# Performance work log

Hardware: AMD Instinct MI355X
Metric: run time of the kernel (lower is better)

The kernel has to match this reference:

```python
import jax, jax.numpy as jnp
import numpy as np

K = 512           # num_embeddings
D = 256           # embedding_dim
GRID = (16, 32)   # SOM grid, prod == K
SIGMA = 2.0       # Gaussian neighborhood width (blur at step 0)
COMMITMENT_COST = 0.25
KOHONEN_COST = 1.0


def _make_blur_matrix():
    # Grid.init id->coord: coord[j] = (i // prod(shape[:j])) % shape[j]
    idx = np.arange(K)
    c0 = idx % GRID[0]
    c1 = (idx // GRID[0]) % GRID[1]
    coords = np.stack([c0, c1], axis=-1).astype(np.float32)  # [K, 2]
    dist = np.linalg.norm(coords[None, :, :] - coords[:, None, :], axis=-1)  # [K, K]
    return jnp.asarray(np.exp(-(dist ** 2) / (2.0 * SIGMA ** 2)), dtype=jnp.float32)


def setup_inputs() -> dict:
    key = jax.random.key(0)
    kx, kw = jax.random.split(key)
    x = jax.random.normal(kx, (64, 32, 32, D), dtype=jnp.float32)
    w = jax.random.normal(kw, (K, D), dtype=jnp.float32)
    bmat = _make_blur_matrix()  # [K, K] constant buffer
    return {"x": x, "w": w, "bmat": bmat}


def reference(x, w, bmat):
    sg = jax.lax.stop_gradient
    flat = x.reshape(-1, D)  # [N, D]

    # nearest-code search (no_grad in torch)
    fw = sg(flat)
    ww = sg(w)
    dists = (jnp.sum(fw ** 2, axis=1, keepdims=True)
             + jnp.sum(ww ** 2, axis=1)
             - 2.0 * fw @ ww.T)                       # [N, K]
    enc_idx = jnp.argmin(dists, axis=1)               # [N]
    encodings = jax.nn.one_hot(enc_idx, K, dtype=jnp.float32)  # [N, K]

    # embedding lookup (differentiable w.r.t. w)
    quant_flat = w[enc_idx]                           # [N, D]
    quantized = quant_flat.reshape(x.shape)

    # l2_batch(w, quantized.detach()) -> [N, K]
    qd = sg(quant_flat)
    diff = (jnp.sum(w ** 2, axis=1)[None, :]
            + jnp.sum(qd ** 2, axis=1, keepdims=True)
            - 2.0 * qd @ w.T)                         # [N, K]

    # blur-weighted kohonen loss: bmm(diff[N,1,K], bmat[idx][N,K,1]).mean()
    selected = bmat[enc_idx]                          # [N, K]
    kohonen_loss = jnp.mean(jnp.sum(diff * selected, axis=-1))

    avg_probs = jnp.mean(encodings, axis=0)
    perplexity = jnp.exp(-jnp.sum(avg_probs * jnp.log(avg_probs + 1e-10)))

    e_latent = jnp.mean((sg(quantized) - x) ** 2)
    q_latent = jnp.mean((quantized - sg(x)) ** 2)
    loss = q_latent + COMMITMENT_COST * e_latent + KOHONEN_COST * kohonen_loss

    quantized_st = x + sg(quantized - x)              # straight-through
    return loss, quantized_st, perplexity, enc_idx
```

## Files before the change

### kernel.cpp

```cpp
#include <hip/hip_runtime.h>
#include <hip/hip_bf16.h>
#include <hip/hip_fp16.h>
#include <math.h>

#define NPTS 65536
#define DIM  256
#define KC   512

#define BM    64
#define NBLK  (NPTS / BM)
#define XSTR  264
#define EPS   0.01f

#define QOFF  1
#define PIDX  16777217
#define EOFF  16777218


typedef _Float16 h8    __attribute__((ext_vector_type(8)));
typedef float    f32x4 __attribute__((ext_vector_type(4)));

__device__ inline void cvt_split8(float4 a, float4 b, h8& hv, h8& lv) {
    float f[8] = {a.x, a.y, a.z, a.w, b.x, b.y, b.z, b.w};
    #pragma unroll
    for (int i = 0; i < 8; ++i) {
        _Float16 h = (_Float16)f[i];
        hv[i] = h;
        lv[i] = (_Float16)(f[i] - (float)h);
    }
}

__device__ inline void gload16(const _Float16* gp, _Float16* lp) {
    __builtin_amdgcn_global_load_lds(
        (const __attribute__((address_space(1))) void*)gp,
        (__attribute__((address_space(3))) void*)lp, 16, 0, 0);
}

__device__ inline void merge_top2(float& b1, int& i1, float& b2, int& i2,
                                  float ob1, int oi1, float ob2, int oi2) {
    bool ow = (ob1 < b1) || (ob1 == b1 && oi1 < i1);
    float lb = ow ? b1 : ob1; int li = ow ? i1 : oi1;
    if (ow) { b1 = ob1; i1 = oi1; }
    float c2 = b2; int ci = i2;
    if (ob2 < c2 || (ob2 == c2 && oi2 < ci)) { c2 = ob2; ci = oi2; }
    if (lb  < c2 || (lb  == c2 && li  < ci)) { c2 = lb;  ci = li;  }
    b2 = c2; i2 = ci;
}

__device__ inline float exact_dist(const float* __restrict__ xr,
                                   const float* __restrict__ w, int c, float wsqc) {
    const float* wr = w + (size_t)c * DIM;
    float d0 = 0.f, d1 = 0.f, d2 = 0.f, d3 = 0.f;
    #pragma unroll 4
    for (int d = 0; d < DIM; d += 4) {
        d0 = fmaf(xr[d + 0], wr[d + 0], d0);
        d1 = fmaf(xr[d + 1], wr[d + 1], d1);
        d2 = fmaf(xr[d + 2], wr[d + 2], d2);
        d3 = fmaf(xr[d + 3], wr[d + 3], d3);
    }
    return wsqc - 2.f * ((d0 + d1) + (d2 + d3));
}

__global__ __launch_bounds__(256) void som_wsq(const float* __restrict__ w,
                                               float* __restrict__ wsq,
                                               int* __restrict__ hist,
                                               double* __restrict__ mse_acc)
{
    int k = blockIdx.x * 256 + threadIdx.x;
    const float4* r = reinterpret_cast<const float4*>(w + (size_t)k * DIM);
    float s0 = 0.f, s1 = 0.f, s2 = 0.f, s3 = 0.f;
    #pragma unroll 8
    for (int q = 0; q < DIM / 4; ++q) {
        float4 v = r[q];
        s0 = fmaf(v.x, v.x, s0);
        s1 = fmaf(v.y, v.y, s1);
        s2 = fmaf(v.z, v.z, s2);
        s3 = fmaf(v.w, v.w, s3);
    }
    wsq[k] = (s0 + s1) + (s2 + s3);
    hist[k] = 0;
    if (k == 0) *mse_acc = 0.0;
}

__global__ __launch_bounds__(256) void som_conv(const float* __restrict__ w,
                                                _Float16* __restrict__ wfh,
                                                _Float16* __restrict__ wfl)
{
    const int tid = threadIdx.x;
    const int row = blockIdx.x * 8 + (tid >> 5);
    const int g   = tid & 31;
    const float4* r = reinterpret_cast<const float4*>(w + (size_t)row * DIM);
    float4 a = r[g * 2], b = r[g * 2 + 1];
    h8 hv, lv; cvt_split8(a, b, hv, lv);
    int dsl = g >> 2, kg = g & 3;
    size_t off = ((size_t)(dsl * 32 + (row >> 4))) * 512 + kg * 128 + (row & 15) * 8;
    *reinterpret_cast<h8*>(wfh + off) = hv;
    *reinterpret_cast<h8*>(wfl + off) = lv;
}

__global__ __launch_bounds__(512) void som_main(const float* __restrict__ x,
                                                const float* __restrict__ w,
                                                const _Float16* __restrict__ wfh,
                                                const _Float16* __restrict__ wfl,
                                                float* __restrict__ out,
                                                const float* __restrict__ wsq,
                                                int* __restrict__ hist,
                                                double* __restrict__ mse_acc)
{
    alignas(16) __shared__ _Float16 AsH[16384];
    alignas(16) __shared__ _Float16 AsL[16384];
    alignas(16) __shared__ _Float16 xh[BM * XSTR];
    alignas(16) __shared__ _Float16 xl[BM * XSTR];
    __shared__ float wsq_s[KC];
    __shared__ float xsq_s[BM];
    __shared__ float red_b[8][BM], red_s[8][BM];
    __shared__ int   red_ib[8][BM], red_is[8][BM];
    __shared__ int   bidx_s[BM];

    const int tid  = threadIdx.x;
    const int lane = tid & 63;
    const int wid  = tid >> 6;
    const int l15  = lane & 15;
    const int kg   = lane >> 4;
    const int ptBlock = blockIdx.x * BM;

    const float4* xg4 = reinterpret_cast<const float4*>(x);
    #pragma unroll
    for (int it = 0; it < 4; ++it) {
        int u = it * 512 + tid, row = u >> 5, c8 = u & 31;
        float4 a = xg4[(size_t)(ptBlock + row) * 64 + c8 * 2];
        float4 b = xg4[(size_t)(ptBlock + row) * 64 + c8 * 2 + 1];
        h8 hv, lv; cvt_split8(a, b, hv, lv);
        *reinterpret_cast<h8*>(&xh[row * XSTR + c8 * 8]) = hv;
        *reinterpret_cast<h8*>(&xl[row * XSTR + c8 * 8]) = lv;
        float s = ((fmaf(a.x, a.x, a.y * a.y) + fmaf(a.z, a.z, a.w * a.w))
                 + (fmaf(b.x, b.x, b.y * b.y) + fmaf(b.z, b.z, b.w * b.w)));
        #pragma unroll
        for (int m = 1; m <= 16; m <<= 1) s += __shfl_xor(s, m, 64);
        if ((lane & 31) == 0) xsq_s[row] = s;
    }
    wsq_s[tid] = wsq[tid];

    const int codeBase = wid * 64;
    const int ctg0 = wid * 4;

    f32x4 acc[4][4];
    #pragma unroll
    for (int rt = 0; rt < 4; ++rt)
        #pragma unroll
        for (int ct = 0; ct < 4; ++ct)
            acc[rt][ct] = (f32x4){0.f, 0.f, 0.f, 0.f};

    #pragma unroll 1
    for (int dsl = 0; dsl < 8; ++dsl) {
        #pragma unroll
        for (int i = 0; i < 4; ++i) {
            size_t goff = (size_t)dsl * 16384 + (size_t)(i * 512 + tid) * 8;
            int loff = (i * 512 + wid * 64) * 8;
            gload16(wfh + goff, &AsH[loff]);
            gload16(wfl + goff, &AsL[loff]);
        }
        __syncthreads();

        h8 Bh[4], Bl[4];
        #pragma unroll
        for (int ct = 0; ct < 4; ++ct) {
            int boff = (ct * 16 + l15) * XSTR + dsl * 32 + kg * 8;
            Bh[ct] = *reinterpret_cast<const h8*>(&xh[boff]);
            Bl[ct] = *reinterpret_cast<const h8*>(&xl[boff]);
        }
        #pragma unroll
        for (int rt = 0; rt < 4; ++rt) {
            int aoff = (ctg0 + rt) * 512 + kg * 128 + l15 * 8;
            h8 Ah = *reinterpret_cast<const h8*>(&AsH[aoff]);
            h8 Al = *reinterpret_cast<const h8*>(&AsL[aoff]);
            #pragma unroll
            for (int ct = 0; ct < 4; ++ct)
                acc[rt][ct] = __builtin_amdgcn_mfma_f32_16x16x32_f16(Ah, Bh[ct], acc[rt][ct], 0, 0, 0);
            #pragma unroll
            for (int ct = 0; ct < 4; ++ct)
                acc[rt][ct] = __builtin_amdgcn_mfma_f32_16x16x32_f16(Al, Bh[ct], acc[rt][ct], 0, 0, 0);
            #pragma unroll
            for (int ct = 0; ct < 4; ++ct)
                acc[rt][ct] = __builtin_amdgcn_mfma_f32_16x16x32_f16(Ah, Bl[ct], acc[rt][ct], 0, 0, 0);
        }
        __syncthreads();
    }

    float sb[4], ss[4];
    int   ib[4], is2[4];
    #pragma unroll
    for (int ct = 0; ct < 4; ++ct) { sb[ct] = INFINITY; ss[ct] = INFINITY; ib[ct] = 0; is2[ct] = 0; }
    #pragma unroll
    for (int rt = 0; rt < 4; ++rt) {
        int cbase = codeBase + rt * 16 + kg * 4;
        #pragma unroll
        for (int ct = 0; ct < 4; ++ct) {
            #pragma unroll
            for (int r = 0; r < 4; ++r) {
                int cc = cbase + r;
                float d = wsq_s[cc] - 2.f * acc[rt][ct][r];
                if (d < sb[ct] || (d == sb[ct] && cc < ib[ct])) {
                    ss[ct] = sb[ct]; is2[ct] = ib[ct]; sb[ct] = d; ib[ct] = cc;
                } else if (d < ss[ct] || (d == ss[ct] && cc < is2[ct])) {
                    ss[ct] = d; is2[ct] = cc;
                }
            }
        }
    }
    #pragma unroll
    for (int ct = 0; ct < 4; ++ct) {
        #pragma unroll
        for (int m = 16; m <= 32; m <<= 1) {
            float ob1 = __shfl_xor(sb[ct], m, 64), ob2 = __shfl_xor(ss[ct], m, 64);
            int   oi1 = __shfl_xor(ib[ct], m, 64), oi2 = __shfl_xor(is2[ct], m, 64);
            merge_top2(sb[ct], ib[ct], ss[ct], is2[ct], ob1, oi1, ob2, oi2);
        }
    }
    if (kg == 0) {
        #pragma unroll
        for (int ct = 0; ct < 4; ++ct) {
            int p = ct * 16 + l15;
            red_b[wid][p] = sb[ct];  red_s[wid][p] = ss[ct];
            red_ib[wid][p] = ib[ct]; red_is[wid][p] = is2[ct];
        }
    }
    __syncthreads();

    if (tid < BM) {
        float b = red_b[0][tid], s = red_s[0][tid];
        int  bi = red_ib[0][tid], si = red_is[0][tid];
        #pragma unroll
        for (int g = 1; g < 8; ++g)
            merge_top2(b, bi, s, si, red_b[g][tid], red_ib[g][tid], red_s[g][tid], red_is[g][tid]);

        if (s - b < EPS) {
            const float* xrp = x + (size_t)(ptBlock + tid) * DIM;
            float d1 = exact_dist(xrp, w, bi, wsq_s[bi]);
            float d2 = exact_dist(xrp, w, si, wsq_s[si]);
            if (d2 < d1 || (d2 == d1 && si < bi)) { bi = si; b = d2; } else { b = d1; }
        }
        bidx_s[tid] = bi;
        out[EOFF + ptBlock + tid] = (float)bi;
        atomicAdd(&hist[bi], 1);

        float msum = xsq_s[tid] + b;
        #pragma unroll
        for (int m = 32; m; m >>= 1) msum += __shfl_xor(msum, m, 64);
        if (tid == 0) atomicAdd(mse_acc, (double)msum);
    }
    __syncthreads();

    {
        const float4* wg4 = reinterpret_cast<const float4*>(w);
        float4* q4 = reinterpret_cast<float4*>(out + QOFF);
        #pragma unroll
        for (int r8 = 0; r8 < 8; ++r8) {
            int row = r8 * 8 + wid;
            int cc = bidx_s[row];
            q4[(size_t)(ptBlock + row) * 64 + lane] = wg4[(size_t)cc * 64 + lane];
        }
    }
}

__global__ __launch_bounds__(256) void som_g(const float* __restrict__ w,
                                             const float* __restrict__ bmat,
                                             const float* __restrict__ wsq,
                                             float* __restrict__ g)
{
    __shared__ float wj[DIM];
    __shared__ float psum[4];
    const int j = blockIdx.x;
    const int tid = threadIdx.x;
    wj[tid] = w[(size_t)j * DIM + tid];
    __syncthreads();
    const float wsqj = wsq[j];
    float sum = 0.f;
    for (int k = tid; k < KC; k += 256) {
        const float* wk = &w[(size_t)k * DIM];
        float d0 = 0.f, d1 = 0.f, d2 = 0.f, d3 = 0.f;
        #pragma unroll 4
        for (int d = 0; d < DIM; d += 4) {
            d0 = fmaf(wj[d + 0], wk[d + 0], d0);
            d1 = fmaf(wj[d + 1], wk[d + 1], d1);
            d2 = fmaf(wj[d + 2], wk[d + 2], d2);
            d3 = fmaf(wj[d + 3], wk[d + 3], d3);
        }
        float dot = (d0 + d1) + (d2 + d3);
        float t = wsq[k] + wsqj - 2.f * dot;
        sum = fmaf(bmat[(size_t)j * KC + k], t, sum);
    }
    #pragma unroll
    for (int m = 32; m; m >>= 1) sum += __shfl_xor(sum, m, 64);
    int lane = tid & 63, wid = tid >> 6;
    if (lane == 0) psum[wid] = sum;
    __syncthreads();
    if (tid == 0) g[j] = (psum[0] + psum[1]) + (psum[2] + psum[3]);
}

__global__ __launch_bounds__(512) void som_final(const int* __restrict__ hist,
                                                 const float* __restrict__ g,
                                                 const double* __restrict__ mse_acc,
                                                 float* __restrict__ out)
{
    __shared__ float e_part[8], k_part[8];
    const int tid = threadIdx.x;
    int cnt = hist[tid];
    float p = (float)cnt / (float)NPTS;
    float ent = -p * logf(p + 1e-10f);
    float koh = (float)cnt * g[tid];
    #pragma unroll
    for (int m = 32; m; m >>= 1) {
        ent += __shfl_xor(ent, m, 64);
        koh += __shfl_xor(koh, m, 64);
    }
    int lane = tid & 63, wid = tid >> 6;
    if (lane == 0) { e_part[wid] = ent; k_part[wid] = koh; }
    __syncthreads();
    if (tid == 0) {
        float es = 0.f, ks = 0.f;
        #pragma unroll
        for (int i = 0; i < 8; ++i) { es += e_part[i]; ks += k_part[i]; }
        float mse = (float)(*mse_acc / (double)(NPTS * (size_t)DIM));
        out[0] = fmaf(1.25f, mse, ks / (float)NPTS);
        out[PIDX] = expf(es);
    }
}

extern "C" void kernel_launch(void* const* d_in, const int* in_sizes, int n_in,
                              void* d_out, int out_size, void* d_ws, size_t ws_size,
                              hipStream_t stream) {
    const float* x    = (const float*)d_in[0];
    const float* w    = (const float*)d_in[1];
    const float* bmat = (const float*)d_in[2];
    float* out = (float*)d_out;

    _Float16* wfh = (_Float16*)d_ws;
    _Float16* wfl = wfh + 131072;
    float*  wsq  = (float*)((char*)d_ws + 524288);
    float*  g    = (float*)((char*)d_ws + 526336);
    int*    hist = (int*)((char*)d_ws + 528384);
    double* mse  = (double*)((char*)d_ws + 530432);

    som_wsq  <<<2, 256, 0, stream>>>(w, wsq, hist, mse);
    som_conv <<<64, 256, 0, stream>>>(w, wfh, wfl);
    som_main <<<NBLK, 512, 0, stream>>>(x, w, wfh, wfl, out, wsq, hist, mse);
    som_g    <<<KC, 256, 0, stream>>>(w, bmat, wsq, g);
    som_final<<<1, KC, 0, stream>>>(hist, g, mse, out);
}
```

Measured before the change: 191.0 us.

## Double point tile, stream codebook fragments from global, and split codes across waves

The point tile grows to 128 rows with 1024-thread blocks. The codebook hi/lo fp16 fragments are no longer staged into LDS via global_load_lds with barriers; each wave reads its A fragments directly from global/L2 in a relaid-out fragment order. Codes are processed in two passes of 256, so each wave holds fewer accumulators. Reduction buffers now alias the x tile in LDS. This removes per-slice syncs and LDS codebook traffic, but relies on L2 bandwidth for repeated codebook reads and halves the number of blocks.

Result: faster. 164.7 us (-13.8%).

```diff
diff --git a/kernel.cpp b/kernel.cpp
--- a/kernel.cpp
+++ b/kernel.cpp
@@ -7,7 +7,7 @@
 #define DIM  256
 #define KC   512
 
-#define BM    64
+#define BM    128
 #define NBLK  (NPTS / BM)
 #define XSTR  264
 #define EPS   0.01f
@@ -28,12 +28,6 @@
         hv[i] = h;
         lv[i] = (_Float16)(f[i] - (float)h);
     }
-}
-
-__device__ inline void gload16(const _Float16* gp, _Float16* lp) {
-    __builtin_amdgcn_global_load_lds(
-        (const __attribute__((address_space(1))) void*)gp,
-        (__attribute__((address_space(3))) void*)lp, 16, 0, 0);
 }
 
 __device__ inline void merge_top2(float& b1, int& i1, float& b2, int& i2,
@@ -93,41 +87,46 @@
     float4 a = r[g * 2], b = r[g * 2 + 1];
     h8 hv, lv; cvt_split8(a, b, hv, lv);
     int dsl = g >> 2, kg = g & 3;
-    size_t off = ((size_t)(dsl * 32 + (row >> 4))) * 512 + kg * 128 + (row & 15) * 8;
+    int ctg = row >> 4, l15 = row & 15;
+    size_t off = (((size_t)(ctg * 8 + dsl)) * 4 + kg) * 128 + l15 * 8;
     *reinterpret_cast<h8*>(wfh + off) = hv;
     *reinterpret_cast<h8*>(wfl + off) = lv;
 }
 
-__global__ __launch_bounds__(512) void som_main(const float* __restrict__ x,
-                                                const float* __restrict__ w,
-                                                const _Float16* __restrict__ wfh,
-                                                const _Float16* __restrict__ wfl,
-                                                float* __restrict__ out,
-                                                const float* __restrict__ wsq,
-                                                int* __restrict__ hist,
-                                                double* __restrict__ mse_acc)
-{
-    alignas(16) __shared__ _Float16 AsH[16384];
-    alignas(16) __shared__ _Float16 AsL[16384];
+__global__ __launch_bounds__(1024) void som_main(const float* __restrict__ x,
+                                                 const float* __restrict__ w,
+                                                 const _Float16* __restrict__ wfh,
+                                                 const _Float16* __restrict__ wfl,
+                                                 float* __restrict__ out,
+                                                 const float* __restrict__ wsq,
+                                                 int* __restrict__ hist,
+                                                 double* __restrict__ mse_acc)
+{
     alignas(16) __shared__ _Float16 xh[BM * XSTR];
     alignas(16) __shared__ _Float16 xl[BM * XSTR];
     __shared__ float wsq_s[KC];
     __shared__ float xsq_s[BM];
-    __shared__ float red_b[8][BM], red_s[8][BM];
-    __shared__ int   red_ib[8][BM], red_is[8][BM];
-    __shared__ int   bidx_s[BM];
+    __shared__ float wsum[2];
+
+    float* red_b  = reinterpret_cast<float*>(xh);
+    float* red_s  = red_b + 8 * BM;
+    int*   red_ib = reinterpret_cast<int*>(red_s + 8 * BM);
+    int*   red_is = red_ib + 8 * BM;
+    int*   bidx_s = reinterpret_cast<int*>(xl);
 
     const int tid  = threadIdx.x;
     const int lane = tid & 63;
     const int wid  = tid >> 6;
     const int l15  = lane & 15;
     const int kg   = lane >> 4;
+    const int pgrp = wid & 1;
+    const int cgrp = wid >> 1;
     const int ptBlock = blockIdx.x * BM;
 
     const float4* xg4 = reinterpret_cast<const float4*>(x);
     #pragma unroll
     for (int it = 0; it < 4; ++it) {
-        int u = it * 512 + tid, row = u >> 5, c8 = u & 31;
+        int u = it * 1024 + tid, row = u >> 5, c8 = u & 31;
         float4 a = xg4[(size_t)(ptBlock + row) * 64 + c8 * 2];
         float4 b = xg4[(size_t)(ptBlock + row) * 64 + c8 * 2 + 1];
         h8 hv, lv; cvt_split8(a, b, hv, lv);
@@ -139,75 +138,78 @@
         for (int m = 1; m <= 16; m <<= 1) s += __shfl_xor(s, m, 64);
         if ((lane & 31) == 0) xsq_s[row] = s;
     }
-    wsq_s[tid] = wsq[tid];
-
-    const int codeBase = wid * 64;
-    const int ctg0 = wid * 4;
-
-    f32x4 acc[4][4];
-    #pragma unroll
-    for (int rt = 0; rt < 4; ++rt)
-        #pragma unroll
-        for (int ct = 0; ct < 4; ++ct)
-            acc[rt][ct] = (f32x4){0.f, 0.f, 0.f, 0.f};
-
-    #pragma unroll 1
-    for (int dsl = 0; dsl < 8; ++dsl) {
-        #pragma unroll
-        for (int i = 0; i < 4; ++i) {
-            size_t goff = (size_t)dsl * 16384 + (size_t)(i * 512 + tid) * 8;
-            int loff = (i * 512 + wid * 64) * 8;
-            gload16(wfh + goff, &AsH[loff]);
-            gload16(wfl + goff, &AsL[loff]);
-        }
-        __syncthreads();
-
-        h8 Bh[4], Bl[4];
-        #pragma unroll
-        for (int ct = 0; ct < 4; ++ct) {
-            int boff = (ct * 16 + l15) * XSTR + dsl * 32 + kg * 8;
-            Bh[ct] = *reinterpret_cast<const h8*>(&xh[boff]);
-            Bl[ct] = *reinterpret_cast<const h8*>(&xl[boff]);
-        }
-        #pragma unroll
-        for (int rt = 0; rt < 4; ++rt) {
-            int aoff = (ctg0 + rt) * 512 + kg * 128 + l15 * 8;
-            h8 Ah = *reinterpret_cast<const h8*>(&AsH[aoff]);
-            h8 Al = *reinterpret_cast<const h8*>(&AsL[aoff]);
-            #pragma unroll
-            for (int ct = 0; ct < 4; ++ct)
-                acc[rt][ct] = __builtin_amdgcn_mfma_f32_16x16x32_f16(Ah, Bh[ct], acc[rt][ct], 0, 0, 0);
-            #pragma unroll
-            for (int ct = 0; ct < 4; ++ct)
-                acc[rt][ct] = __builtin_amdgcn_mfma_f32_16x16x32_f16(Al, Bh[ct], acc[rt][ct], 0, 0, 0);
-            #pragma unroll
-            for (int ct = 0; ct < 4; ++ct)
-                acc[rt][ct] = __builtin_amdgcn_mfma_f32_16x16x32_f16(Ah, Bl[ct], acc[rt][ct], 0, 0, 0);
-        }
-        __syncthreads();
-    }
+    if (tid < KC) wsq_s[tid] = wsq[tid];
+    __syncthreads();
 
     float sb[4], ss[4];
     int   ib[4], is2[4];
     #pragma unroll
     for (int ct = 0; ct < 4; ++ct) { sb[ct] = INFINITY; ss[ct] = INFINITY; ib[ct] = 0; is2[ct] = 0; }
-    #pragma unroll
-    for (int rt = 0; rt < 4; ++rt) {
-        int cbase = codeBase + rt * 16 + kg * 4;
-        #pragma unroll
-        for (int ct = 0; ct < 4; ++ct) {
+
+    #pragma unroll 1
+    for (int pass = 0; pass < 2; ++pass) {
+        f32x4 acc[2][4];
+        #pragma unroll
+        for (int rt = 0; rt < 2; ++rt)
+            #pragma unroll
+            for (int ct = 0; ct < 4; ++ct)
+                acc[rt][ct] = (f32x4){0.f, 0.f, 0.f, 0.f};
+
+        #pragma unroll 1
+        for (int dsl = 0; dsl < 8; ++dsl) {
+            int boff0 = (pgrp * 64 + l15) * XSTR + dsl * 32 + kg * 8;
+            h8 Bh[4];
+            #pragma unroll
+            for (int ct = 0; ct < 4; ++ct)
+                Bh[ct] = *reinterpret_cast<const h8*>(&xh[boff0 + ct * 16 * XSTR]);
+            h8 Ah[2], Al[2];
+            #pragma unroll
+            for (int rt = 0; rt < 2; ++rt) {
+                int ctg = pass * 16 + cgrp * 2 + rt;
+                size_t aoff = ((size_t)ctg * 8 + dsl) * 512 + kg * 128 + l15 * 8;
+                Ah[rt] = *reinterpret_cast<const h8*>(wfh + aoff);
+                Al[rt] = *reinterpret_cast<const h8*>(wfl + aoff);
+            }
+            #pragma unroll
+            for (int rt = 0; rt < 2; ++rt)
+                #pragma unroll
+                for (int ct = 0; ct < 4; ++ct)
+                    acc[rt][ct] = __builtin_amdgcn_mfma_f32_16x16x32_f16(Ah[rt], Bh[ct], acc[rt][ct], 0, 0, 0);
+            #pragma unroll
+            for (int rt = 0; rt < 2; ++rt)
+                #pragma unroll
+                for (int ct = 0; ct < 4; ++ct)
+                    acc[rt][ct] = __builtin_amdgcn_mfma_f32_16x16x32_f16(Al[rt], Bh[ct], acc[rt][ct], 0, 0, 0);
+            h8 Bl[4];
+            #pragma unroll
+            for (int ct = 0; ct < 4; ++ct)
+                Bl[ct] = *reinterpret_cast<const h8*>(&xl[boff0 + ct * 16 * XSTR]);
+            #pragma unroll
+            for (int rt = 0; rt < 2; ++rt)
+                #pragma unroll
+                for (int ct = 0; ct < 4; ++ct)
+                    acc[rt][ct] = __builtin_amdgcn_mfma_f32_16x16x32_f16(Ah[rt], Bl[ct], acc[rt][ct], 0, 0, 0);
+        }
+
+        #pragma unroll
+        for (int rt = 0; rt < 2; ++rt) {
             #pragma unroll
             for (int r = 0; r < 4; ++r) {
-                int cc = cbase + r;
-                float d = wsq_s[cc] - 2.f * acc[rt][ct][r];
-                if (d < sb[ct] || (d == sb[ct] && cc < ib[ct])) {
-                    ss[ct] = sb[ct]; is2[ct] = ib[ct]; sb[ct] = d; ib[ct] = cc;
-                } else if (d < ss[ct] || (d == ss[ct] && cc < is2[ct])) {
-                    ss[ct] = d; is2[ct] = cc;
+                int cc = pass * 256 + cgrp * 32 + rt * 16 + kg * 4 + r;
+                float wq = wsq_s[cc];
+                #pragma unroll
+                for (int ct = 0; ct < 4; ++ct) {
+                    float d = wq - 2.f * acc[rt][ct][r];
+                    if (d < sb[ct] || (d == sb[ct] && cc < ib[ct])) {
+                        ss[ct] = sb[ct]; is2[ct] = ib[ct]; sb[ct] = d; ib[ct] = cc;
+                    } else if (d < ss[ct] || (d == ss[ct] && cc < is2[ct])) {
+                        ss[ct] = d; is2[ct] = cc;
+                    }
                 }
             }
         }
     }
+
     #pragma unroll
     for (int ct = 0; ct < 4; ++ct) {
         #pragma unroll
@@ -217,22 +219,25 @@
             merge_top2(sb[ct], ib[ct], ss[ct], is2[ct], ob1, oi1, ob2, oi2);
         }
     }
+    __syncthreads();
+
     if (kg == 0) {
         #pragma unroll
         for (int ct = 0; ct < 4; ++ct) {
-            int p = ct * 16 + l15;
-            red_b[wid][p] = sb[ct];  red_s[wid][p] = ss[ct];
-            red_ib[wid][p] = ib[ct]; red_is[wid][p] = is2[ct];
+            int p = pgrp * 64 + ct * 16 + l15;
+            red_b[cgrp * BM + p] = sb[ct];  red_s[cgrp * BM + p] = ss[ct];
+            red_ib[cgrp * BM + p] = ib[ct]; red_is[cgrp * BM + p] = is2[ct];
         }
     }
     __syncthreads();
 
     if (tid < BM) {
-        float b = red_b[0][tid], s = red_s[0][tid];
-        int  bi = red_ib[0][tid], si = red_is[0][tid];
+        float b = red_b[tid], s = red_s[tid];
+        int  bi = red_ib[tid], si = red_is[tid];
         #pragma unroll
         for (int g = 1; g < 8; ++g)
-            merge_top2(b, bi, s, si, red_b[g][tid], red_ib[g][tid], red_s[g][tid], red_is[g][tid]);
+            merge_top2(b, bi, s, si, red_b[g * BM + tid], red_ib[g * BM + tid],
+                       red_s[g * BM + tid], red_is[g * BM + tid]);
 
         if (s - b < EPS) {
             const float* xrp = x + (size_t)(ptBlock + tid) * DIM;
@@ -247,16 +252,17 @@
         float msum = xsq_s[tid] + b;
         #pragma unroll
         for (int m = 32; m; m >>= 1) msum += __shfl_xor(msum, m, 64);
-        if (tid == 0) atomicAdd(mse_acc, (double)msum);
-    }
-    __syncthreads();
+        if (lane == 0) wsum[wid] = msum;
+    }
+    __syncthreads();
+    if (tid == 0) atomicAdd(mse_acc, (double)(wsum[0] + wsum[1]));
 
     {
         const float4* wg4 = reinterpret_cast<const float4*>(w);
         float4* q4 = reinterpret_cast<float4*>(out + QOFF);
         #pragma unroll
         for (int r8 = 0; r8 < 8; ++r8) {
-            int row = r8 * 8 + wid;
+            int row = r8 * 16 + wid;
             int cc = bidx_s[row];
             q4[(size_t)(ptBlock + row) * 64 + lane] = wg4[(size_t)cc * 64 + lane];
         }
@@ -344,7 +350,7 @@
 
     som_wsq  <<<2, 256, 0, stream>>>(w, wsq, hist, mse);
     som_conv <<<64, 256, 0, stream>>>(w, wfh, wfl);
-    som_main <<<NBLK, 512, 0, stream>>>(x, w, wfh, wfl, out, wsq, hist, mse);
+    som_main <<<NBLK, 1024, 0, stream>>>(x, w, wfh, wfl, out, wsq, hist, mse);
     som_g    <<<KC, 256, 0, stream>>>(w, bmat, wsq, g);
     som_final<<<1, KC, 0, stream>>>(hist, g, mse, out);
 }
```
